# Performance work log

Measured on AMD Instinct MI355X. Metric: run time of the kernel, lower is better.

Reference implementation:

```python
import jax, jax.numpy as jnp
import numpy as np

B, N, D, S, H, ITERS = 64, 4096, 128, 7, 256, 3
EPS = 1e-8

def layer_norm(x, g, b):
    m = jnp.mean(x, axis=-1, keepdims=True)
    v = jnp.var(x, axis=-1, keepdims=True)
    return (x - m) * jax.lax.rsqrt(v + 1e-5) * g + b

def setup_inputs() -> dict:
    key = jax.random.key(0)
    ks = jax.random.split(key, 16)
    lin = lambda k, o, i: jax.random.normal(k, (o, i), jnp.float32) / np.sqrt(i)
    return {
        "embeddings": jax.random.normal(ks[0], (B, N, D), jnp.float32),
        "noise": jax.random.normal(ks[1], (B, S, D), jnp.float32),
        "slots_mu": jax.random.normal(ks[2], (1, 1, D), jnp.float32),
        "slots_sigma": jax.random.uniform(ks[3], (1, 1, D), jnp.float32),
        "Wk": lin(ks[4], D, D), "bk": jnp.zeros((D,), jnp.float32),
        "Wq": lin(ks[5], D, D), "bq": jnp.zeros((D,), jnp.float32),
        "Wv": lin(ks[6], D, D), "bv": jnp.zeros((D,), jnp.float32),
        "W_ih": lin(ks[7], 3 * D, D), "W_hh": lin(ks[8], 3 * D, D),
        "b_ih": jnp.zeros((3 * D,), jnp.float32), "b_hh": jnp.zeros((3 * D,), jnp.float32),
        "W1": lin(ks[9], H, D), "b1": jnp.zeros((H,), jnp.float32),
        "W2": lin(ks[10], D, H), "b2": jnp.zeros((D,), jnp.float32),
        "ln_in_g": jnp.ones((D,), jnp.float32), "ln_in_b": jnp.zeros((D,), jnp.float32),
        "ln_s_g": jnp.ones((D,), jnp.float32), "ln_s_b": jnp.zeros((D,), jnp.float32),
        "ln_ff_g": jnp.ones((D,), jnp.float32), "ln_ff_b": jnp.zeros((D,), jnp.float32),
    }

def reference(embeddings, noise, slots_mu, slots_sigma, Wk, bk, Wq, bq, Wv, bv,
              W_ih, W_hh, b_ih, b_hh, W1, b1, W2, b2,
              ln_in_g, ln_in_b, ln_s_g, ln_s_b, ln_ff_g, ln_ff_b):
    # slot init: normal(mu, sigma) with fixed noise
    slots = slots_mu + slots_sigma * noise  # [B,S,D]
    emb = layer_norm(embeddings, ln_in_g, ln_in_b)
    keys = emb @ Wk.T + bk      # [B,N,D]
    values = emb @ Wv.T + bv    # [B,N,D]
    for _ in range(ITERS):
        slots_prev = slots
        q = layer_norm(slots, ln_s_g, ln_s_b) @ Wq.T + bq  # [B,S,D]
        dots = jnp.einsum('bid,bjd->bij', q, keys)          # [B,S,N]
        attn = jax.nn.softmax(dots, axis=-1) + EPS
        attn = attn / jnp.sum(attn, axis=-1, keepdims=True)
        updates = jnp.einsum('bjd,bij->bid', values, attn)  # [B,S,D]
        # GRUCell (pytorch gate order: r, z, n)
        x = updates.reshape(-1, D)
        h = slots_prev.reshape(-1, D)
        gi = x @ W_ih.T + b_ih
        gh = h @ W_hh.T + b_hh
        gi_r, gi_z, gi_n = jnp.split(gi, 3, axis=-1)
        gh_r, gh_z, gh_n = jnp.split(gh, 3, axis=-1)
        r = jax.nn.sigmoid(gi_r + gh_r)
        z = jax.nn.sigmoid(gi_z + gh_z)
        n = jnp.tanh(gi_n + r * gh_n)
        slots = ((1.0 - z) * n + z * h).reshape(B, S, D)
        ff = jax.nn.relu(layer_norm(slots, ln_ff_g, ln_ff_b) @ W1.T + b1) @ W2.T + b2
        slots = slots + ff
    return slots
```

## Files before the change

kernel.cpp:

```cpp
#include <hip/hip_runtime.h>
#include <math.h>

#define B_ 64
#define N_ 4096
#define D_ 128
#define S_ 7
#define H_ 256
#define ITERS_ 3
#define AP 132
#define NCHUNK 8

__device__ __forceinline__ float dot4(float4 a, float4 b) {
  return a.x * b.x + a.y * b.y + a.z * b.z + a.w * b.w;
}
__device__ __forceinline__ float4 ld4(const float* p) {
  return *reinterpret_cast<const float4*>(p);
}

__global__ void k_init(const float* __restrict__ noise, const float* __restrict__ mu,
                       const float* __restrict__ sigma, float* __restrict__ slots) {
  int idx = blockIdx.x * 256 + threadIdx.x;
  int d = idx & 127;
  slots[idx] = mu[d] + sigma[d] * noise[idx];
}

__global__ void k_wt(const float* __restrict__ W, float* __restrict__ out, int R, int C) {
  int idx = blockIdx.x * 256 + threadIdx.x;
  if (idx >= R * C) return;
  int d = idx / C, i = idx - d * C;
  out[(((i >> 2) * R + d) << 2) + (i & 3)] = W[idx];
}

__global__ __launch_bounds__(128) void k_q(
    const float* __restrict__ slots, const float* __restrict__ Wq, const float* __restrict__ bq,
    const float* __restrict__ g, const float* __restrict__ b,
    const float* __restrict__ Wk, float* __restrict__ qp) {
  __shared__ __align__(16) float lns[AP];
  __shared__ __align__(16) float qs2[AP];
  __shared__ float red[4];
  int row = blockIdx.x;
  int d = threadIdx.x;
  float x = slots[row * D_ + d];
  float s1 = x, s2 = x * x;
#pragma unroll
  for (int off = 32; off >= 1; off >>= 1) { s1 += __shfl_down(s1, off); s2 += __shfl_down(s2, off); }
  if ((d & 63) == 0) { red[(d >> 6) * 2] = s1; red[(d >> 6) * 2 + 1] = s2; }
  __syncthreads();
  float sum = red[0] + red[2], sumsq = red[1] + red[3];
  float mean = sum * (1.f / 128.f);
  float var = sumsq * (1.f / 128.f) - mean * mean;
  float rs = rsqrtf(var + 1e-5f);
  lns[d] = (x - mean) * rs * g[d] + b[d];
  __syncthreads();
  const float* w = Wq + d * D_;
  float acc = bq[d];
  for (int i4 = 0; i4 < D_; i4 += 4) acc += dot4(*reinterpret_cast<const float4*>(&lns[i4]), ld4(w + i4));
  qs2[d] = acc;
  __syncthreads();
  float qpa = 0.f;
#pragma unroll 4
  for (int dd = 0; dd < D_; dd++) qpa += qs2[dd] * Wk[dd * D_ + d];
  qp[row * D_ + d] = qpa;
}

__global__ __launch_bounds__(256) void k_attn(
    const float* __restrict__ qpbuf, const float* __restrict__ emb,
    const float* __restrict__ lng, const float* __restrict__ lnb,
    float* __restrict__ partialA, float* __restrict__ partialM, float* __restrict__ partialS) {
  __shared__ __align__(16) float vt[64 * AP];
  __shared__ float red[28 * 64];
  __shared__ float pt[7 * 64];
  __shared__ float sm[7], ssum[7], tmax[7];
  int t = threadIdx.x;
  int b = blockIdx.x >> 3, jc = blockIdx.x & (NCHUNK - 1);

  if (t < 7) { sm[t] = -1e30f; ssum[t] = 0.f; }

  int j = t & 63, g = t >> 6;
  int gu = __builtin_amdgcn_readfirstlane(g);
  const float* qb = qpbuf + (long)(b * 7) * D_ + gu * 32;
  int d4 = (t & 31) * 4, jg = t >> 5;
  int ln_i4 = (t & 31) * 4;
  int ln_r8 = t >> 5;
  float4 gv = ld4(&lng[ln_i4]);
  float4 bv4 = ld4(&lnb[ln_i4]);

  float acc[7][4];
#pragma unroll
  for (int s = 0; s < 7; s++)
#pragma unroll
    for (int c = 0; c < 4; c++) acc[s][c] = 0.f;
  __syncthreads();

  for (int sub = 0; sub < 8; sub++) {
    int j0 = jc * 512 + sub * 64;
#pragma unroll
    for (int u = 0; u < 8; u++) {
      int row = u * 8 + ln_r8;
      float4 x = ld4(&emb[((long)b * N_ + j0 + row) * D_ + ln_i4]);
      float s1 = x.x + x.y + x.z + x.w;
      float s2 = dot4(x, x);
#pragma unroll
      for (int off = 16; off >= 1; off >>= 1) {
        s1 += __shfl_xor(s1, off, 32);
        s2 += __shfl_xor(s2, off, 32);
      }
      float mean = s1 * (1.f / 128.f);
      float var = s2 * (1.f / 128.f) - mean * mean;
      float rs = rsqrtf(var + 1e-5f);
      float4 o;
      o.x = (x.x - mean) * rs * gv.x + bv4.x;
      o.y = (x.y - mean) * rs * gv.y + bv4.y;
      o.z = (x.z - mean) * rs * gv.z + bv4.z;
      o.w = (x.w - mean) * rs * gv.w + bv4.w;
      *reinterpret_cast<float4*>(&vt[row * AP + ln_i4]) = o;
    }
    __syncthreads();

    float acc7[7];
#pragma unroll
    for (int s = 0; s < 7; s++) acc7[s] = 0.f;
#pragma unroll
    for (int st = 0; st < 8; st++) {
      float4 kv = *reinterpret_cast<const float4*>(&vt[j * AP + gu * 32 + st * 4]);
#pragma unroll
      for (int s = 0; s < 7; s++) {
        float4 qv = ld4(qb + s * D_ + st * 4);
        acc7[s] += dot4(kv, qv);
      }
    }
#pragma unroll
    for (int s = 0; s < 7; s++) red[(g * 7 + s) * 64 + j] = acc7[s];
    __syncthreads();

    for (int pp = t; pp < 448; pp += 256) {
      int s = pp >> 6, jj = pp & 63;
      pt[pp] = red[s * 64 + jj] + red[(7 + s) * 64 + jj] +
               red[(14 + s) * 64 + jj] + red[(21 + s) * 64 + jj];
    }
    __syncthreads();

    if (t < 224) {
      int s = t >> 5, i = t & 31;
      float m = fmaxf(pt[s * 64 + i], pt[s * 64 + 32 + i]);
#pragma unroll
      for (int off = 16; off >= 1; off >>= 1) m = fmaxf(m, __shfl_down(m, off, 32));
      if ((t & 31) == 0) tmax[s] = m;
    }
    __syncthreads();

#pragma unroll
    for (int s = 0; s < 7; s++) {
      float mnew = fmaxf(sm[s], tmax[s]);
      float scl = __expf(sm[s] - mnew);
#pragma unroll
      for (int c = 0; c < 4; c++) acc[s][c] *= scl;
    }
    for (int pp = t; pp < 448; pp += 256) {
      int s = pp >> 6;
      float mnew = fmaxf(sm[s], tmax[s]);
      pt[pp] = __expf(pt[pp] - mnew);
    }
    __syncthreads();

    if (t < 224) {
      int s = t >> 5, i = t & 31;
      float ssub = pt[s * 64 + i] + pt[s * 64 + 32 + i];
#pragma unroll
      for (int off = 16; off >= 1; off >>= 1) ssub += __shfl_down(ssub, off, 32);
      if ((t & 31) == 0) {
        float mnew = fmaxf(sm[s], tmax[s]);
        float scl = __expf(sm[s] - mnew);
        ssum[s] = ssum[s] * scl + ssub;
        sm[s] = mnew;
      }
    }

#pragma unroll
    for (int jl = 0; jl < 8; jl++) {
      int jj = jg * 8 + jl;
      float4 vv = *reinterpret_cast<const float4*>(&vt[jj * AP + d4]);
#pragma unroll
      for (int s = 0; s < 7; s++) {
        float e = pt[s * 64 + jj];
        acc[s][0] += e * vv.x; acc[s][1] += e * vv.y;
        acc[s][2] += e * vv.z; acc[s][3] += e * vv.w;
      }
    }
    __syncthreads();
  }

  float* redf = vt;
#pragma unroll
  for (int s = 0; s < 7; s++)
    *reinterpret_cast<float4*>(&redf[(jg * 7 + s) * 128 + d4]) =
        make_float4(acc[s][0], acc[s][1], acc[s][2], acc[s][3]);
  __syncthreads();
  for (int pp = t; pp < 896; pp += 256) {
    int s = pp >> 7, d = pp & 127;
    float x = 0.f;
#pragma unroll
    for (int g2 = 0; g2 < 8; g2++) x += redf[(g2 * 7 + s) * 128 + d];
    partialA[((long)(b * NCHUNK + jc) * 7 + s) * 128 + d] = x;
  }
  if (t < 7) {
    partialM[(b * NCHUNK + jc) * 7 + t] = sm[t];
    partialS[(b * NCHUNK + jc) * 7 + t] = ssum[t];
  }
}

__global__ __launch_bounds__(256) void k_gruffq(
    const float* __restrict__ partialA, const float* __restrict__ partialM,
    const float* __restrict__ partialS, float* __restrict__ slots,
    const float* __restrict__ wtV, const float* __restrict__ bv,
    const float* __restrict__ wtIH, const float* __restrict__ wtHH,
    const float* __restrict__ bih, const float* __restrict__ bhh,
    const float* __restrict__ wt1, const float* __restrict__ b1,
    const float* __restrict__ wt2, const float* __restrict__ b2,
    const float* __restrict__ gff, const float* __restrict__ bff,
    const float* __restrict__ lsg, const float* __restrict__ lsb,
    const float* __restrict__ wtQ, const float* __restrict__ bq,
    const float* __restrict__ Wk, float* __restrict__ qp, int compute_q) {
  __shared__ __align__(16) float us[AP];
  __shared__ __align__(16) float xs[AP];
  __shared__ __align__(16) float hs[AP];
  __shared__ __align__(16) float nss[AP];
  __shared__ __align__(16) float lns[AP];
  __shared__ __align__(16) float sn[AP];
  __shared__ __align__(16) float qv[AP];
  __shared__ __align__(16) float h1s[H_];
  __shared__ __align__(16) float g6[6 * 128];
  __shared__ __align__(16) float pp[2 * 128];
  __shared__ float den2[2];
  __shared__ float red2[2];
  int t = threadIdx.x;
  int d = t & 127, h = t >> 7;
  int blk = blockIdx.x;
  int b = blk / 7, s = blk % 7;

  float mg = -1e30f;
#pragma unroll
  for (int c = 0; c < NCHUNK; c++) mg = fmaxf(mg, partialM[(b * NCHUNK + c) * 7 + s]);
  float up = 0.f, den = 0.f;
#pragma unroll
  for (int cc = 0; cc < NCHUNK / 2; cc++) {
    int c = h * (NCHUNK / 2) + cc;
    float w = __expf(partialM[(b * NCHUNK + c) * 7 + s] - mg);
    den += w * partialS[(b * NCHUNK + c) * 7 + s];
    up += w * partialA[((long)(b * NCHUNK + c) * 7 + s) * 128 + d];
  }
  pp[h * 128 + d] = up;
  if (d == 0) den2[h] = den;
  if (h == 1) hs[d] = slots[blk * D_ + d];
  __syncthreads();
  if (h == 0) us[d] = (pp[d] + pp[128 + d]) / (den2[0] + den2[1]);
  __syncthreads();

  {
    float acc = 0.f;
#pragma unroll
    for (int k = 0; k < 16; k++) {
      int i4 = h * 16 + k;
      acc += dot4(*reinterpret_cast<const float4*>(&us[i4 * 4]),
                  ld4(wtV + (i4 * 128 + d) * 4));
    }
    pp[h * 128 + d] = acc;
  }
  __syncthreads();
  if (h == 0) xs[d] = bv[d] + pp[d] + pp[128 + d];
  __syncthreads();

  {
    const float* wt = (h == 0) ? wtIH : wtHH;
    const float* bias = (h == 0) ? bih : bhh;
    const float* vec = (h == 0) ? xs : hs;
    float a0 = bias[d], a1 = bias[128 + d], a2 = bias[256 + d];
#pragma unroll
    for (int i4 = 0; i4 < 32; i4++) {
      float4 v = *reinterpret_cast<const float4*>(&vec[i4 * 4]);
      a0 += dot4(v, ld4(wt + (i4 * 384 + d) * 4));
      a1 += dot4(v, ld4(wt + (i4 * 384 + 128 + d) * 4));
      a2 += dot4(v, ld4(wt + (i4 * 384 + 256 + d) * 4));
    }
    g6[(h * 3 + 0) * 128 + d] = a0;
    g6[(h * 3 + 1) * 128 + d] = a1;
    g6[(h * 3 + 2) * 128 + d] = a2;
  }
  __syncthreads();
  if (h == 0) {
    float gir = g6[d], giz = g6[128 + d], gin = g6[256 + d];
    float ghr = g6[384 + d], ghz = g6[512 + d], ghn = g6[640 + d];
    float r = 1.f / (1.f + __expf(-(gir + ghr)));
    float z = 1.f / (1.f + __expf(-(giz + ghz)));
    float n = tanhf(gin + r * ghn);
    nss[d] = (1.f - z) * n + z * hs[d];
  }
  __syncthreads();

  if (t < 64) {
    float v0 = nss[t], v1 = nss[t + 64];
    float s1 = v0 + v1, s2 = v0 * v0 + v1 * v1;
#pragma unroll
    for (int off = 32; off >= 1; off >>= 1) { s1 += __shfl_down(s1, off); s2 += __shfl_down(s2, off); }
    if (t == 0) { red2[0] = s1; red2[1] = s2; }
  }
  __syncthreads();
  {
    float mean = red2[0] * (1.f / 128.f);
    float var = red2[1] * (1.f / 128.f) - mean * mean;
    float rs = rsqrtf(var + 1e-5f);
    if (h == 0) lns[d] = (nss[d] - mean) * rs * gff[d] + bff[d];
  }
  __syncthreads();

  {
    float a = b1[t];
#pragma unroll
    for (int i4 = 0; i4 < 32; i4++)
      a += dot4(*reinterpret_cast<const float4*>(&lns[i4 * 4]),
                ld4(wt1 + (i4 * 256 + t) * 4));
    h1s[t] = fmaxf(a, 0.f);
  }
  __syncthreads();

  {
    float acc = 0.f;
#pragma unroll
    for (int k = 0; k < 32; k++) {
      int h4 = h * 32 + k;
      acc += dot4(*reinterpret_cast<const float4*>(&h1s[h4 * 4]),
                  ld4(wt2 + (h4 * 128 + d) * 4));
    }
    pp[h * 128 + d] = acc;
  }
  __syncthreads();
  if (h == 0) {
    float out = nss[d] + b2[d] + pp[d] + pp[128 + d];
    sn[d] = out;
    slots[blk * D_ + d] = out;
  }
  __syncthreads();

  if (!compute_q) return;

  if (t < 64) {
    float v0 = sn[t], v1 = sn[t + 64];
    float s1 = v0 + v1, s2 = v0 * v0 + v1 * v1;
#pragma unroll
    for (int off = 32; off >= 1; off >>= 1) { s1 += __shfl_down(s1, off); s2 += __shfl_down(s2, off); }
    if (t == 0) { red2[0] = s1; red2[1] = s2; }
  }
  __syncthreads();
  {
    float mean = red2[0] * (1.f / 128.f);
    float var = red2[1] * (1.f / 128.f) - mean * mean;
    float rs = rsqrtf(var + 1e-5f);
    if (h == 0) lns[d] = (sn[d] - mean) * rs * lsg[d] + lsb[d];
  }
  __syncthreads();
  {
    float acc = 0.f;
#pragma unroll
    for (int k = 0; k < 16; k++) {
      int i4 = h * 16 + k;
      acc += dot4(*reinterpret_cast<const float4*>(&lns[i4 * 4]),
                  ld4(wtQ + (i4 * 128 + d) * 4));
    }
    pp[h * 128 + d] = acc;
  }
  __syncthreads();
  if (h == 0) qv[d] = bq[d] + pp[d] + pp[128 + d];
  __syncthreads();
  {
    float acc = 0.f;
    const float* wc = Wk + h * 64 * D_ + d;
#pragma unroll 4
    for (int dd = 0; dd < 64; dd++) acc += qv[h * 64 + dd] * wc[dd * D_];
    pp[h * 128 + d] = acc;
  }
  __syncthreads();
  if (h == 0) qp[blk * D_ + d] = pp[d] + pp[128 + d];
}

extern "C" void kernel_launch(void* const* d_in, const int* in_sizes, int n_in,
                              void* d_out, int out_size, void* d_ws, size_t ws_size,
                              hipStream_t stream) {
  const float* emb   = (const float*)d_in[0];
  const float* noise = (const float*)d_in[1];
  const float* mu    = (const float*)d_in[2];
  const float* sigma = (const float*)d_in[3];
  const float* Wk = (const float*)d_in[4];  const float* bk = (const float*)d_in[5];
  const float* Wq = (const float*)d_in[6];  const float* bq = (const float*)d_in[7];
  const float* Wv = (const float*)d_in[8];  const float* bv = (const float*)d_in[9];
  const float* Wih = (const float*)d_in[10]; const float* Whh = (const float*)d_in[11];
  const float* bih = (const float*)d_in[12]; const float* bhh = (const float*)d_in[13];
  const float* W1 = (const float*)d_in[14];  const float* b1 = (const float*)d_in[15];
  const float* W2 = (const float*)d_in[16];  const float* b2 = (const float*)d_in[17];
  const float* lin_g = (const float*)d_in[18]; const float* lin_b = (const float*)d_in[19];
  const float* ls_g  = (const float*)d_in[20]; const float* ls_b  = (const float*)d_in[21];
  const float* lff_g = (const float*)d_in[22]; const float* lff_b = (const float*)d_in[23];
  (void)bk;

  float* slots = (float*)d_out;
  float* qp       = (float*)d_ws;
  float* partialA = qp + (size_t)B_ * S_ * D_;
  float* partialM = partialA + (size_t)B_ * NCHUNK * S_ * D_;
  float* partialS = partialM + (size_t)B_ * NCHUNK * S_;
  float* wtV  = partialS + (size_t)B_ * NCHUNK * S_;
  float* wtIH = wtV + 16384;
  float* wtHH = wtIH + 49152;
  float* wtQ  = wtHH + 49152;
  float* wt1  = wtQ + 16384;
  float* wt2  = wt1 + 32768;

  k_init<<<224, 256, 0, stream>>>(noise, mu, sigma, slots);
  k_wt<<<64, 256, 0, stream>>>(Wv, wtV, 128, 128);
  k_wt<<<192, 256, 0, stream>>>(Wih, wtIH, 384, 128);
  k_wt<<<192, 256, 0, stream>>>(Whh, wtHH, 384, 128);
  k_wt<<<64, 256, 0, stream>>>(Wq, wtQ, 128, 128);
  k_wt<<<128, 256, 0, stream>>>(W1, wt1, 256, 128);
  k_wt<<<128, 256, 0, stream>>>(W2, wt2, 128, 256);
  k_q<<<448, 128, 0, stream>>>(slots, Wq, bq, ls_g, ls_b, Wk, qp);
  for (int it = 0; it < ITERS_; it++) {
    k_attn<<<B_ * NCHUNK, 256, 0, stream>>>(qp, emb, lin_g, lin_b, partialA, partialM, partialS);
    k_gruffq<<<448, 256, 0, stream>>>(partialA, partialM, partialS, slots, wtV, bv,
                                      wtIH, wtHH, bih, bhh, wt1, b1, wt2, b2, lff_g, lff_b,
                                      ls_g, ls_b, wtQ, bq, Wk, qp, it < ITERS_ - 1 ? 1 : 0);
  }
}
```

Measured before the change: 506.9 us.

## Restructure attention kernel to per-row-group online softmax in registers

The attention kernel now has each 16-lane group stream 32 embedding rows. It applies layernorm, computes the 7 slot scores with shuffle reductions and keeps a per-group online softmax with accumulators held in registers. This removes the shared-memory tiles for the normalized rows, the staged score reductions and the many block barriers inside each sub-tile. The 16 per-group partial states are merged at the end with max rescaling. The trade-off is higher register pressure (56 accumulators plus 14 float4 queries), which could lower occupancy, and more exp work per row.

Result: faster. 444.5 us (-12.3%).

```diff
diff --git a/kernel.cpp b/kernel.cpp
--- a/kernel.cpp
+++ b/kernel.cpp
@@ -67,145 +67,120 @@
     const float* __restrict__ qpbuf, const float* __restrict__ emb,
     const float* __restrict__ lng, const float* __restrict__ lnb,
     float* __restrict__ partialA, float* __restrict__ partialM, float* __restrict__ partialS) {
-  __shared__ __align__(16) float vt[64 * AP];
-  __shared__ float red[28 * 64];
-  __shared__ float pt[7 * 64];
-  __shared__ float sm[7], ssum[7], tmax[7];
+  __shared__ __align__(16) float lacc[16 * 7 * 128];
+  __shared__ float lm[16 * 7], lsm[16 * 7];
+  __shared__ float wgt[7 * 16];
+  __shared__ float mstar[7];
   int t = threadIdx.x;
   int b = blockIdx.x >> 3, jc = blockIdx.x & (NCHUNK - 1);
-
-  if (t < 7) { sm[t] = -1e30f; ssum[t] = 0.f; }
-
-  int j = t & 63, g = t >> 6;
-  int gu = __builtin_amdgcn_readfirstlane(g);
-  const float* qb = qpbuf + (long)(b * 7) * D_ + gu * 32;
-  int d4 = (t & 31) * 4, jg = t >> 5;
-  int ln_i4 = (t & 31) * 4;
-  int ln_r8 = t >> 5;
-  float4 gv = ld4(&lng[ln_i4]);
-  float4 bv4 = ld4(&lnb[ln_i4]);
-
-  float acc[7][4];
+  int lane = t & 63;
+  int gid = (t >> 6) * 4 + (lane >> 4);
+  int li = lane & 15;
+  int i8 = li * 8;
+
+  float4 q0[7], q1[7];
+#pragma unroll
+  for (int s = 0; s < 7; s++) {
+    q0[s] = ld4(&qpbuf[(b * 7 + s) * D_ + i8]);
+    q1[s] = ld4(&qpbuf[(b * 7 + s) * D_ + i8 + 4]);
+  }
+  float4 gv0 = ld4(&lng[i8]), gv1 = ld4(&lng[i8 + 4]);
+  float4 bv0 = ld4(&lnb[i8]), bv1 = ld4(&lnb[i8 + 4]);
+
+  float acc[7][8];
 #pragma unroll
   for (int s = 0; s < 7; s++)
 #pragma unroll
-    for (int c = 0; c < 4; c++) acc[s][c] = 0.f;
-  __syncthreads();
-
-  for (int sub = 0; sub < 8; sub++) {
-    int j0 = jc * 512 + sub * 64;
-#pragma unroll
-    for (int u = 0; u < 8; u++) {
-      int row = u * 8 + ln_r8;
-      float4 x = ld4(&emb[((long)b * N_ + j0 + row) * D_ + ln_i4]);
-      float s1 = x.x + x.y + x.z + x.w;
-      float s2 = dot4(x, x);
-#pragma unroll
-      for (int off = 16; off >= 1; off >>= 1) {
-        s1 += __shfl_xor(s1, off, 32);
-        s2 += __shfl_xor(s2, off, 32);
-      }
-      float mean = s1 * (1.f / 128.f);
-      float var = s2 * (1.f / 128.f) - mean * mean;
-      float rs = rsqrtf(var + 1e-5f);
-      float4 o;
-      o.x = (x.x - mean) * rs * gv.x + bv4.x;
-      o.y = (x.y - mean) * rs * gv.y + bv4.y;
-      o.z = (x.z - mean) * rs * gv.z + bv4.z;
-      o.w = (x.w - mean) * rs * gv.w + bv4.w;
-      *reinterpret_cast<float4*>(&vt[row * AP + ln_i4]) = o;
-    }
-    __syncthreads();
-
-    float acc7[7];
-#pragma unroll
-    for (int s = 0; s < 7; s++) acc7[s] = 0.f;
-#pragma unroll
-    for (int st = 0; st < 8; st++) {
-      float4 kv = *reinterpret_cast<const float4*>(&vt[j * AP + gu * 32 + st * 4]);
-#pragma unroll
-      for (int s = 0; s < 7; s++) {
-        float4 qv = ld4(qb + s * D_ + st * 4);
-        acc7[s] += dot4(kv, qv);
-      }
-    }
-#pragma unroll
-    for (int s = 0; s < 7; s++) red[(g * 7 + s) * 64 + j] = acc7[s];
-    __syncthreads();
-
-    for (int pp = t; pp < 448; pp += 256) {
-      int s = pp >> 6, jj = pp & 63;
-      pt[pp] = red[s * 64 + jj] + red[(7 + s) * 64 + jj] +
-               red[(14 + s) * 64 + jj] + red[(21 + s) * 64 + jj];
-    }
-    __syncthreads();
-
-    if (t < 224) {
-      int s = t >> 5, i = t & 31;
-      float m = fmaxf(pt[s * 64 + i], pt[s * 64 + 32 + i]);
-#pragma unroll
-      for (int off = 16; off >= 1; off >>= 1) m = fmaxf(m, __shfl_down(m, off, 32));
-      if ((t & 31) == 0) tmax[s] = m;
-    }
-    __syncthreads();
-
+    for (int c = 0; c < 8; c++) acc[s][c] = 0.f;
+  float m[7], ssum[7];
+#pragma unroll
+  for (int s = 0; s < 7; s++) { m[s] = -1e30f; ssum[s] = 0.f; }
+
+  const float* src = emb + ((long)b * N_ + jc * 512 + gid * 32) * D_ + i8;
+  float4 x0 = ld4(src), x1 = ld4(src + 4);
+  for (int i = 0; i < 32; i++) {
+    float4 c0 = x0, c1 = x1;
+    if (i < 31) {
+      x0 = ld4(src + (i + 1) * D_);
+      x1 = ld4(src + (i + 1) * D_ + 4);
+    }
+    float s1 = c0.x + c0.y + c0.z + c0.w + c1.x + c1.y + c1.z + c1.w;
+    float s2 = dot4(c0, c0) + dot4(c1, c1);
+#pragma unroll
+    for (int off = 8; off >= 1; off >>= 1) {
+      s1 += __shfl_xor(s1, off, 16);
+      s2 += __shfl_xor(s2, off, 16);
+    }
+    float mean = s1 * (1.f / 128.f);
+    float var = s2 * (1.f / 128.f) - mean * mean;
+    float rs = rsqrtf(var + 1e-5f);
+    float4 o0, o1;
+    o0.x = (c0.x - mean) * rs * gv0.x + bv0.x;
+    o0.y = (c0.y - mean) * rs * gv0.y + bv0.y;
+    o0.z = (c0.z - mean) * rs * gv0.z + bv0.z;
+    o0.w = (c0.w - mean) * rs * gv0.w + bv0.w;
+    o1.x = (c1.x - mean) * rs * gv1.x + bv1.x;
+    o1.y = (c1.y - mean) * rs * gv1.y + bv1.y;
+    o1.z = (c1.z - mean) * rs * gv1.z + bv1.z;
+    o1.w = (c1.w - mean) * rs * gv1.w + bv1.w;
 #pragma unroll
     for (int s = 0; s < 7; s++) {
-      float mnew = fmaxf(sm[s], tmax[s]);
-      float scl = __expf(sm[s] - mnew);
-#pragma unroll
-      for (int c = 0; c < 4; c++) acc[s][c] *= scl;
-    }
-    for (int pp = t; pp < 448; pp += 256) {
-      int s = pp >> 6;
-      float mnew = fmaxf(sm[s], tmax[s]);
-      pt[pp] = __expf(pt[pp] - mnew);
-    }
-    __syncthreads();
-
-    if (t < 224) {
-      int s = t >> 5, i = t & 31;
-      float ssub = pt[s * 64 + i] + pt[s * 64 + 32 + i];
-#pragma unroll
-      for (int off = 16; off >= 1; off >>= 1) ssub += __shfl_down(ssub, off, 32);
-      if ((t & 31) == 0) {
-        float mnew = fmaxf(sm[s], tmax[s]);
-        float scl = __expf(sm[s] - mnew);
-        ssum[s] = ssum[s] * scl + ssub;
-        sm[s] = mnew;
-      }
-    }
-
-#pragma unroll
-    for (int jl = 0; jl < 8; jl++) {
-      int jj = jg * 8 + jl;
-      float4 vv = *reinterpret_cast<const float4*>(&vt[jj * AP + d4]);
-#pragma unroll
-      for (int s = 0; s < 7; s++) {
-        float e = pt[s * 64 + jj];
-        acc[s][0] += e * vv.x; acc[s][1] += e * vv.y;
-        acc[s][2] += e * vv.z; acc[s][3] += e * vv.w;
-      }
-    }
-    __syncthreads();
-  }
-
-  float* redf = vt;
-#pragma unroll
-  for (int s = 0; s < 7; s++)
-    *reinterpret_cast<float4*>(&redf[(jg * 7 + s) * 128 + d4]) =
+      float p = dot4(o0, q0[s]) + dot4(o1, q1[s]);
+#pragma unroll
+      for (int off = 8; off >= 1; off >>= 1) p += __shfl_xor(p, off, 16);
+      float mnew = fmaxf(m[s], p);
+      float scl = __expf(m[s] - mnew);
+      float e = __expf(p - mnew);
+      m[s] = mnew;
+      ssum[s] = ssum[s] * scl + e;
+      acc[s][0] = acc[s][0] * scl + e * o0.x;
+      acc[s][1] = acc[s][1] * scl + e * o0.y;
+      acc[s][2] = acc[s][2] * scl + e * o0.z;
+      acc[s][3] = acc[s][3] * scl + e * o0.w;
+      acc[s][4] = acc[s][4] * scl + e * o1.x;
+      acc[s][5] = acc[s][5] * scl + e * o1.y;
+      acc[s][6] = acc[s][6] * scl + e * o1.z;
+      acc[s][7] = acc[s][7] * scl + e * o1.w;
+    }
+  }
+
+#pragma unroll
+  for (int s = 0; s < 7; s++) {
+    *reinterpret_cast<float4*>(&lacc[(gid * 7 + s) * 128 + i8]) =
         make_float4(acc[s][0], acc[s][1], acc[s][2], acc[s][3]);
-  __syncthreads();
+    *reinterpret_cast<float4*>(&lacc[(gid * 7 + s) * 128 + i8 + 4]) =
+        make_float4(acc[s][4], acc[s][5], acc[s][6], acc[s][7]);
+  }
+  if (li == 0) {
+#pragma unroll
+    for (int s = 0; s < 7; s++) { lm[gid * 7 + s] = m[s]; lsm[gid * 7 + s] = ssum[s]; }
+  }
+  __syncthreads();
+  if (t < 7) {
+    float mx = -1e30f;
+#pragma unroll
+    for (int g2 = 0; g2 < 16; g2++) mx = fmaxf(mx, lm[g2 * 7 + t]);
+    mstar[t] = mx;
+  }
+  __syncthreads();
+  if (t < 112) {
+    int s = t >> 4, g2 = t & 15;
+    wgt[s * 16 + g2] = __expf(lm[g2 * 7 + s] - mstar[s]);
+  }
+  __syncthreads();
+  if (t < 7) {
+    float dsum = 0.f;
+#pragma unroll
+    for (int g2 = 0; g2 < 16; g2++) dsum += wgt[t * 16 + g2] * lsm[g2 * 7 + t];
+    partialM[(b * NCHUNK + jc) * 7 + t] = mstar[t];
+    partialS[(b * NCHUNK + jc) * 7 + t] = dsum;
+  }
   for (int pp = t; pp < 896; pp += 256) {
     int s = pp >> 7, d = pp & 127;
     float x = 0.f;
 #pragma unroll
-    for (int g2 = 0; g2 < 8; g2++) x += redf[(g2 * 7 + s) * 128 + d];
+    for (int g2 = 0; g2 < 16; g2++) x += wgt[s * 16 + g2] * lacc[(g2 * 7 + s) * 128 + d];
     partialA[((long)(b * NCHUNK + jc) * 7 + s) * 128 + d] = x;
-  }
-  if (t < 7) {
-    partialM[(b * NCHUNK + jc) * 7 + t] = sm[t];
-    partialS[(b * NCHUNK + jc) * 7 + t] = ssum[t];
   }
 }
 
```
